# Kernel tuning notes

Hardware: AMD Instinct MI355X
Metric: run time of the kernel (lower is better)

The kernel has to match this reference:

```python
import jax, jax.numpy as jnp
import numpy as np

EMBED_DIM = 1024
NUM_HEADS = 16
HEAD_DIM = EMBED_DIM // NUM_HEADS


def setup_inputs() -> dict:
    key = jax.random.key(0)
    ks = jax.random.split(key, 9)
    B, S, D = 2, 2048, EMBED_DIM
    scale = 1.0 / np.sqrt(D)
    x = jax.random.normal(ks[0], (B, S, D), dtype=jnp.float32)
    # Linear params (torch nn.Linear: y = x @ W.T + b); store W as [out, in]
    Wq = jax.random.normal(ks[1], (D, D), dtype=jnp.float32) * scale
    bq = jnp.zeros((D,), dtype=jnp.float32)
    Wk = jax.random.normal(ks[2], (D, D), dtype=jnp.float32) * scale
    bk = jnp.zeros((D,), dtype=jnp.float32)
    Wv = jax.random.normal(ks[3], (D, D), dtype=jnp.float32) * scale
    bv = jnp.zeros((D,), dtype=jnp.float32)
    Wo = jax.random.normal(ks[4], (D, D), dtype=jnp.float32) * scale
    bo = jnp.zeros((D,), dtype=jnp.float32)
    return {"x": x, "Wq": Wq, "bq": bq, "Wk": Wk, "bk": bk,
            "Wv": Wv, "bv": bv, "Wo": Wo, "bo": bo}


def reference(x, Wq, bq, Wk, bk, Wv, bv, Wo, bo):
    B, S, D = x.shape
    H, Hd = NUM_HEADS, HEAD_DIM
    scaling = Hd ** -0.5
    # projections (torch Linear: x @ W.T + b)
    q = (x @ Wq.T + bq).reshape(B, S, H, Hd).transpose(0, 2, 1, 3)  # [B,H,S,Hd]
    k = (x @ Wk.T + bk).reshape(B, S, H, Hd).transpose(0, 2, 1, 3)
    v = (x @ Wv.T + bv).reshape(B, S, H, Hd).transpose(0, 2, 1, 3)
    # full score matrix, as in the original (no flash tiling)
    scores = jnp.einsum('bhqd,bhkd->bhqk', q, k) * scaling  # [B,H,S,S]
    attn = jax.nn.softmax(scores, axis=-1)
    # dropout is identity in eval mode
    out = jnp.einsum('bhqk,bhkd->bhqd', attn, v)  # [B,H,S,Hd]
    out = out.transpose(0, 2, 1, 3).reshape(B, S, D)
    return out @ Wo.T + bo
```

## Files before the change

### kernel.cpp

```cpp
#include <hip/hip_runtime.h>
#include <stdint.h>

typedef unsigned short u16;
typedef short short8 __attribute__((ext_vector_type(8)));
typedef short bh4 __attribute__((ext_vector_type(4)));
typedef float f32x4 __attribute__((ext_vector_type(4)));

__device__ __forceinline__ u16 f2bf_fast(float f) {
  union { float f; uint32_t u; } x;
  x.f = f;
  return (u16)((x.u + 0x8000u) >> 16);
}

__device__ __forceinline__ uint32_t pack2bf(float lo, float hi) {
  union { float f; uint32_t u; } a, b;
  a.f = lo; b.f = hi;
  return __builtin_amdgcn_perm(b.u + 0x8000u, a.u + 0x8000u, 0x07060302u);
}

__device__ __forceinline__ float bf2f(uint32_t u) {
  union { uint32_t u; float f; } x;
  x.u = u << 16;
  return x.f;
}

__device__ __forceinline__ void gload_lds16(const void* g, void* l) {
  __builtin_amdgcn_global_load_lds(
      (const __attribute__((address_space(1))) void*)g,
      (__attribute__((address_space(3))) void*)l, 16, 0, 0);
}

__device__ __forceinline__ f32x4 mfma16(short8 a, short8 b, f32x4 c) {
  return __builtin_amdgcn_mfma_f32_16x16x32_bf16(a, b, c, 0, 0, 0);
}

__device__ __forceinline__ f32x4 pv_mfma(bh4 a, bh4 b, f32x4 c) {
#if defined(__AMDGCN__) || defined(__HIP_DEVICE_COMPILE__)
  return __builtin_amdgcn_mfma_f32_16x16x16bf16_1k(a, b, c, 0, 0, 0);
#else
  (void)a; (void)b;
  return c;
#endif
}

__device__ __forceinline__ short8 ldfrag(const u16* base, int tile, int kc,
                                         int lane) {
  return *(const short8*)(base + ((((tile << 5) + kc) << 6) + lane) * 8);
}

#define QSCALE 0.18033688011112042f

__global__ void pack_all(const float* __restrict__ x, const float* __restrict__ wq,
                         const float* __restrict__ wk, const float* __restrict__ wv,
                         const float* __restrict__ wo, u16* __restrict__ xp,
                         u16* __restrict__ wp) {
  const int gi = blockIdx.x * 256 + threadIdx.x;
  const int lane = gi & 63;
  const int kc = (gi >> 6) & 31;
  const int rt = gi >> 11;
  const int col = kc * 32 + (lane >> 4) * 8;
  const float* src;
  int row;
  if (rt < 256) {
    src = x;
    row = rt * 16 + (lane & 15);
  } else {
    const int wti = rt - 256;
    const int widx = wti >> 6;
    src = (widx == 0) ? wq : (widx == 1) ? wk : (widx == 2) ? wv : wo;
    row = (wti & 63) * 16 + (lane & 15);
  }
  const float4* p = (const float4*)(src + (size_t)row * 1024 + col);
  const float4 v0 = p[0], v1 = p[1];
  uint4 o;
  o.x = pack2bf(v0.x, v0.y);
  o.y = pack2bf(v0.z, v0.w);
  o.z = pack2bf(v1.x, v1.y);
  o.w = pack2bf(v1.z, v1.w);
  u16* dst = (rt < 256) ? xp : wp;
  const int og = (rt < 256) ? gi : gi - 524288;
  ((uint4*)dst)[og] = o;
}

__global__ __launch_bounds__(256, 3) void proj_qkv(
    const u16* __restrict__ xp, const u16* __restrict__ wp,
    const float* __restrict__ bq, const float* __restrict__ bk,
    const float* __restrict__ bv, u16* __restrict__ qw, u16* __restrict__ kw,
    u16* __restrict__ vw) {
  const int gid = blockIdx.x * 4 + (threadIdx.x >> 6);
  const int lane = threadIdx.x & 63;
  const int quad = lane >> 4, l15 = lane & 15;
  const bool isQK = gid < 2048;
  int at0, bt0, bm, bn;
  const u16 *Ap, *Bp;
  if (isQK) {
    bn = gid >> 6; bm = gid & 63;
    Ap = xp; at0 = bm * 4;
    Bp = wp; bt0 = bn * 4;
  } else {
    const int h = gid - 2048;
    bn = h & 63; bm = h >> 6;
    Ap = wp; at0 = 128 + bm * 4;
    Bp = xp; bt0 = bn * 4;
  }

  f32x4 acc[4][4] = {};
  short8 af[2][4], bf[2][4];
#pragma unroll
  for (int mt = 0; mt < 4; ++mt) af[0][mt] = ldfrag(Ap, at0 + mt, 0, lane);
#pragma unroll
  for (int nt = 0; nt < 4; ++nt) bf[0][nt] = ldfrag(Bp, bt0 + nt, 0, lane);

#pragma unroll 4
  for (int kc = 0; kc < 32; ++kc) {
    const int cur = kc & 1, nxt = cur ^ 1;
    if (kc < 31) {
#pragma unroll
      for (int mt = 0; mt < 4; ++mt)
        af[nxt][mt] = ldfrag(Ap, at0 + mt, kc + 1, lane);
#pragma unroll
      for (int nt = 0; nt < 4; ++nt)
        bf[nxt][nt] = ldfrag(Bp, bt0 + nt, kc + 1, lane);
    }
#pragma unroll
    for (int mt = 0; mt < 4; ++mt)
#pragma unroll
      for (int nt = 0; nt < 4; ++nt)
        acc[mt][nt] = mfma16(af[cur][mt], bf[cur][nt], acc[mt][nt]);
  }

#pragma unroll
  for (int nt = 0; nt < 4; ++nt) {
    const int n = bn * 64 + nt * 16 + l15;
#pragma unroll
    for (int mt = 0; mt < 4; ++mt)
#pragma unroll
      for (int r = 0; r < 4; ++r) {
        const int m = bm * 64 + mt * 16 + quad * 4 + r;
        const float a = acc[mt][nt][r];
        if (isQK) {
          const bool isQ = (bn < 16);
          const int nn = isQ ? n : n - 1024;
          const float v = isQ ? (a + bq[nn]) * QSCALE : a + bk[nn];
          u16* op = isQ ? qw : kw;
          const int b = m >> 11, s = m & 2047, hh = nn >> 6, d = nn & 63;
          op[((size_t)((b * 16 + hh) * 2048 + s)) * 64 + d] = f2bf_fast(v);
        } else {
          const float v = a + bv[m];
          const int b = n >> 11, s = n & 2047;
          vw[((size_t)(b * 1024 + m)) * 2048 + s] = f2bf_fast(v);
        }
      }
  }
}

__global__ __launch_bounds__(256) void attn_kernel(
    const u16* __restrict__ Q, const u16* __restrict__ Kt,
    const u16* __restrict__ Vt, u16* __restrict__ op0, u16* __restrict__ op1,
    float* __restrict__ lp) {
  __shared__ __align__(16) u16 Sm[16384];
  const int tid = threadIdx.x, lane = tid & 63, w = tid >> 6;
  const int quad = lane >> 4, l15 = lane & 15;
  const int qt = blockIdx.x;
  const int bh = blockIdx.y >> 1;
  const int ks = blockIdx.y & 1;

  const char* Qb = (const char*)(Q + ((size_t)bh * 2048 + qt * 128) * 64);
  const char* Kb = (const char*)(Kt + ((size_t)bh * 2048 + ks * 1024) * 64);
  const char* Vb = (const char*)(Vt + (size_t)bh * 64 * 2048 + ks * 1024);

  auto stageKV = [&](int kt, int b) {
    u16* Kl = Sm + b * 4096;
    u16* Vl = Sm + 8192 + b * 4096;
#pragma unroll
    for (int i = 0; i < 2; ++i) {
      const int G = (w * 2 + i) * 64 + lane;
      const int r = G >> 3, sl = G & 7;
      gload_lds16(Kb + (size_t)(kt * 64 + r) * 128 + ((sl ^ (r & 7)) * 16),
                  &Kl[G * 8]);
      gload_lds16(Vb + (size_t)r * 4096 + kt * 128 + ((sl ^ (r & 7)) * 16),
                  &Vl[G * 8]);
    }
  };

#pragma unroll
  for (int i = 0; i < 4; ++i) {
    const int G = (w * 4 + i) * 64 + lane;
    const int row = G >> 3, sl = G & 7;
    u16* qdst = (G < 512) ? (Sm + 4096) : (Sm + 12288);
    gload_lds16(Qb + (size_t)row * 128 + ((sl ^ (row & 7)) * 16),
                &qdst[(G & 511) * 8]);
  }
  stageKV(0, 0);
  __syncthreads();

  const u16* qreg = (w < 2) ? (Sm + 4096) : (Sm + 12288);
  const int qr0 = (w & 1) * 32;
  short8 aq[2][2];
#pragma unroll
  for (int mt = 0; mt < 2; ++mt)
#pragma unroll
    for (int kc = 0; kc < 2; ++kc)
      aq[mt][kc] = *(const short8*)&qreg[(qr0 + mt * 16 + l15) * 64 +
                                         (((kc * 4 + quad) ^ (l15 & 7)) * 8)];
  __syncthreads();

  f32x4 ot[4][2] = {};
  float lsum[2] = {};

  for (int kt = 0; kt < 16; ++kt) {
    const int buf = kt & 1;
    if (kt < 15) stageKV(kt + 1, buf ^ 1);
    const u16* Kl = Sm + buf * 4096;
    const u16* Vl = Sm + 8192 + buf * 4096;

    f32x4 st[2][4] = {};
#pragma unroll
    for (int kc = 0; kc < 2; ++kc)
#pragma unroll
      for (int ntk = 0; ntk < 4; ++ntk) {
        short8 kf = *(const short8*)&Kl[(ntk * 16 + l15) * 64 +
                                        (((kc * 4 + quad) ^ (l15 & 7)) * 8)];
        st[0][ntk] = mfma16(kf, aq[0][kc], st[0][ntk]);
        st[1][ntk] = mfma16(kf, aq[1][kc], st[1][ntk]);
      }

    bh4 bp[2][4];
#pragma unroll
    for (int mt = 0; mt < 2; ++mt)
#pragma unroll
      for (int ntk = 0; ntk < 4; ++ntk) {
        const float e0 = __builtin_amdgcn_exp2f(st[mt][ntk][0]);
        const float e1 = __builtin_amdgcn_exp2f(st[mt][ntk][1]);
        const float e2 = __builtin_amdgcn_exp2f(st[mt][ntk][2]);
        const float e3 = __builtin_amdgcn_exp2f(st[mt][ntk][3]);
        lsum[mt] += (e0 + e1) + (e2 + e3);
        union { uint32_t u[2]; bh4 s; } pb;
        pb.u[0] = pack2bf(e0, e1);
        pb.u[1] = pack2bf(e2, e3);
        bp[mt][ntk] = pb.s;
      }

#pragma unroll
    for (int ntk = 0; ntk < 4; ++ntk) {
      const int swz = ((ntk * 2 + (quad >> 1)) ^ (l15 & 7)) * 8 + (quad & 1) * 4;
#pragma unroll
      for (int ntd = 0; ntd < 4; ++ntd) {
        bh4 vf = *(const bh4*)&Vl[(ntd * 16 + l15) * 64 + swz];
        ot[ntd][0] = pv_mfma(vf, bp[0][ntk], ot[ntd][0]);
        ot[ntd][1] = pv_mfma(vf, bp[1][ntk], ot[ntd][1]);
      }
    }
    if (kt < 15) __syncthreads();
  }

  const int b = bh >> 4, h = bh & 15;
  u16* op = ks ? op1 : op0;
#pragma unroll
  for (int mt = 0; mt < 2; ++mt) {
    float l = lsum[mt];
    l += __shfl_xor(l, 16);
    l += __shfl_xor(l, 32);
    const int srow = qt * 128 + w * 32 + mt * 16 + l15;
    if (quad == 0) lp[((size_t)(ks * 32 + bh)) * 2048 + srow] = l;
    const int rt = b * 128 + qt * 8 + w * 2 + mt;
#pragma unroll
    for (int ntd = 0; ntd < 4; ++ntd) {
      const int kc = h * 2 + (ntd >> 1);
      const int lnq = ((ntd & 1) * 2 + (quad >> 1)) & 3;
      const int j0 = (quad & 1) * 4;
      uint2 ov;
      ov.x = pack2bf(ot[ntd][mt][0], ot[ntd][mt][1]);
      ov.y = pack2bf(ot[ntd][mt][2], ot[ntd][mt][3]);
      *(uint2*)(op + ((size_t)((rt * 32 + kc) * 64 + lnq * 16 + l15)) * 8 + j0) = ov;
    }
  }
}

__global__ void attn_combine(const u16* __restrict__ op0,
                             const u16* __restrict__ op1,
                             const float* __restrict__ lp,
                             u16* __restrict__ awp) {
  const int g = blockIdx.x * 256 + threadIdx.x;
  const int ln = g & 63;
  const int kc = (g >> 6) & 31;
  const int rt = g >> 11;
  const int row = rt * 16 + (ln & 15);
  const int b = row >> 11, s = row & 2047;
  const int h = kc >> 1;
  const int lidx = (b * 16 + h) * 2048 + s;
  const float inv = __builtin_amdgcn_rcpf(lp[lidx] + lp[lidx + 65536]);
  const uint4 a0 = ((const uint4*)op0)[g];
  const uint4 a1 = ((const uint4*)op1)[g];
  uint4 o;
  o.x = pack2bf((bf2f(a0.x) + bf2f(a1.x)) * inv,
                (bf2f(a0.x >> 16) + bf2f(a1.x >> 16)) * inv);
  o.y = pack2bf((bf2f(a0.y) + bf2f(a1.y)) * inv,
                (bf2f(a0.y >> 16) + bf2f(a1.y >> 16)) * inv);
  o.z = pack2bf((bf2f(a0.z) + bf2f(a1.z)) * inv,
                (bf2f(a0.z >> 16) + bf2f(a1.z >> 16)) * inv);
  o.w = pack2bf((bf2f(a0.w) + bf2f(a1.w)) * inv,
                (bf2f(a0.w >> 16) + bf2f(a1.w >> 16)) * inv);
  ((uint4*)awp)[g] = o;
}

__global__ __launch_bounds__(256, 3) void out_proj(const u16* __restrict__ awp,
                                                   const u16* __restrict__ wp,
                                                   const float* __restrict__ bo,
                                                   float* __restrict__ out) {
  const int gid = blockIdx.x * 4 + (threadIdx.x >> 6);
  const int lane = threadIdx.x & 63;
  const int quad = lane >> 4, l15 = lane & 15;
  const int bm = gid & 63, bnn = gid >> 6;
  const int at0 = bm * 4, bt0 = 192 + bnn * 2;

  f32x4 acc[4][2] = {};
  short8 af[2][4], bf[2][2];
#pragma unroll
  for (int mt = 0; mt < 4; ++mt) af[0][mt] = ldfrag(awp, at0 + mt, 0, lane);
#pragma unroll
  for (int nt = 0; nt < 2; ++nt) bf[0][nt] = ldfrag(wp, bt0 + nt, 0, lane);

#pragma unroll 4
  for (int kc = 0; kc < 32; ++kc) {
    const int cur = kc & 1, nxt = cur ^ 1;
    if (kc < 31) {
#pragma unroll
      for (int mt = 0; mt < 4; ++mt)
        af[nxt][mt] = ldfrag(awp, at0 + mt, kc + 1, lane);
#pragma unroll
      for (int nt = 0; nt < 2; ++nt)
        bf[nxt][nt] = ldfrag(wp, bt0 + nt, kc + 1, lane);
    }
#pragma unroll
    for (int mt = 0; mt < 4; ++mt)
#pragma unroll
      for (int nt = 0; nt < 2; ++nt)
        acc[mt][nt] = mfma16(af[cur][mt], bf[cur][nt], acc[mt][nt]);
  }

#pragma unroll
  for (int nt = 0; nt < 2; ++nt) {
    const int n = bnn * 32 + nt * 16 + l15;
    const float bb = bo[n];
#pragma unroll
    for (int mt = 0; mt < 4; ++mt)
#pragma unroll
      for (int r = 0; r < 4; ++r) {
        const int m = bm * 64 + mt * 16 + quad * 4 + r;
        out[(size_t)m * 1024 + n] = acc[mt][nt][r] + bb;
      }
  }
}

extern "C" void kernel_launch(void* const* d_in, const int* in_sizes, int n_in,
                              void* d_out, int out_size, void* d_ws, size_t ws_size,
                              hipStream_t stream) {
  const float* x  = (const float*)d_in[0];
  const float* Wq = (const float*)d_in[1];
  const float* bq = (const float*)d_in[2];
  const float* Wk = (const float*)d_in[3];
  const float* bk = (const float*)d_in[4];
  const float* Wv = (const float*)d_in[5];
  const float* bv = (const float*)d_in[6];
  const float* Wo = (const float*)d_in[7];
  const float* bo = (const float*)d_in[8];

  const size_t M4 = (size_t)4 * 1024 * 1024;
  u16* xp  = (u16*)d_ws;
  u16* wp  = xp + M4;
  u16* qw  = wp + M4;
  u16* kw  = qw + M4;
  u16* vw  = kw + M4;
  u16* op1 = vw + M4;
  u16* awp = op1 + M4;
  float* lp = (float*)(awp + M4);
  u16* op0 = xp;

  pack_all<<<4096, 256, 0, stream>>>(x, Wq, Wk, Wv, Wo, xp, wp);

  proj_qkv<<<768, 256, 0, stream>>>(xp, wp, bq, bk, bv, qw, kw, vw);

  attn_kernel<<<dim3(16, 64), 256, 0, stream>>>(qw, kw, vw, op0, op1, lp);

  attn_combine<<<2048, 256, 0, stream>>>(op0, op1, lp, awp);

  out_proj<<<512, 256, 0, stream>>>(awp, wp, bo, (float*)d_out);
}
```

Baseline: 208.6 us.

## Use 16x16x32 MFMA for PV via lane shuffles and XCD-aware GEMM block mapping

```diff
diff --git a/kernel.cpp b/kernel.cpp
--- a/kernel.cpp
+++ b/kernel.cpp
@@ -3,7 +3,6 @@
 
 typedef unsigned short u16;
 typedef short short8 __attribute__((ext_vector_type(8)));
-typedef short bh4 __attribute__((ext_vector_type(4)));
 typedef float f32x4 __attribute__((ext_vector_type(4)));
 
 __device__ __forceinline__ u16 f2bf_fast(float f) {
@@ -32,15 +31,6 @@
 
 __device__ __forceinline__ f32x4 mfma16(short8 a, short8 b, f32x4 c) {
   return __builtin_amdgcn_mfma_f32_16x16x32_bf16(a, b, c, 0, 0, 0);
-}
-
-__device__ __forceinline__ f32x4 pv_mfma(bh4 a, bh4 b, f32x4 c) {
-#if defined(__AMDGCN__) || defined(__HIP_DEVICE_COMPILE__)
-  return __builtin_amdgcn_mfma_f32_16x16x16bf16_1k(a, b, c, 0, 0, 0);
-#else
-  (void)a; (void)b;
-  return c;
-#endif
 }
 
 __device__ __forceinline__ short8 ldfrag(const u16* base, int tile, int kc,
@@ -87,19 +77,25 @@
     const float* __restrict__ bq, const float* __restrict__ bk,
     const float* __restrict__ bv, u16* __restrict__ qw, u16* __restrict__ kw,
     u16* __restrict__ vw) {
-  const int gid = blockIdx.x * 4 + (threadIdx.x >> 6);
+  const int wv2 = threadIdx.x >> 6;
   const int lane = threadIdx.x & 63;
   const int quad = lane >> 4, l15 = lane & 15;
-  const bool isQK = gid < 2048;
+  const int xcd = blockIdx.x & 7;
+  const int bidx = blockIdx.x >> 3;
+  const int xq = xcd >> 1, xh = xcd & 1;
+  const bool isQK = bidx < 64;
   int at0, bt0, bm, bn;
   const u16 *Ap, *Bp;
   if (isQK) {
-    bn = gid >> 6; bm = gid & 63;
+    const int q = bidx;
+    bn = xh * 16 + (q & 15);
+    bm = xq * 16 + (q >> 4) * 4 + wv2;
     Ap = xp; at0 = bm * 4;
     Bp = wp; bt0 = bn * 4;
   } else {
-    const int h = gid - 2048;
-    bn = h & 63; bm = h >> 6;
+    const int v = bidx - 64;
+    bn = xq * 16 + (v & 15);
+    bm = xh * 8 + (v >> 4) * 4 + wv2;
     Ap = wp; at0 = 128 + bm * 4;
     Bp = xp; bt0 = bn * 4;
   }
@@ -164,6 +160,7 @@
   const int qt = blockIdx.x;
   const int bh = blockIdx.y >> 1;
   const int ks = blockIdx.y & 1;
+  const int sl = (l15 & 3) | ((l15 >> 1) & 4) | ((l15 << 1) & 8);
 
   const char* Qb = (const char*)(Q + ((size_t)bh * 2048 + qt * 128) * 64);
   const char* Kb = (const char*)(Kt + ((size_t)bh * 2048 + ks * 1024) * 64);
@@ -175,10 +172,10 @@
 #pragma unroll
     for (int i = 0; i < 2; ++i) {
       const int G = (w * 2 + i) * 64 + lane;
-      const int r = G >> 3, sl = G & 7;
-      gload_lds16(Kb + (size_t)(kt * 64 + r) * 128 + ((sl ^ (r & 7)) * 16),
+      const int r = G >> 3, slw = G & 7;
+      gload_lds16(Kb + (size_t)(kt * 64 + r) * 128 + ((slw ^ (r & 7)) * 16),
                   &Kl[G * 8]);
-      gload_lds16(Vb + (size_t)r * 4096 + kt * 128 + ((sl ^ (r & 7)) * 16),
+      gload_lds16(Vb + (size_t)r * 4096 + kt * 128 + ((slw ^ (r & 7)) * 16),
                   &Vl[G * 8]);
     }
   };
@@ -186,9 +183,9 @@
 #pragma unroll
   for (int i = 0; i < 4; ++i) {
     const int G = (w * 4 + i) * 64 + lane;
-    const int row = G >> 3, sl = G & 7;
+    const int row = G >> 3, slw = G & 7;
     u16* qdst = (G < 512) ? (Sm + 4096) : (Sm + 12288);
-    gload_lds16(Qb + (size_t)row * 128 + ((sl ^ (row & 7)) * 16),
+    gload_lds16(Qb + (size_t)row * 128 + ((slw ^ (row & 7)) * 16),
                 &qdst[(G & 511) * 8]);
   }
   stageKV(0, 0);
@@ -219,13 +216,13 @@
     for (int kc = 0; kc < 2; ++kc)
 #pragma unroll
       for (int ntk = 0; ntk < 4; ++ntk) {
-        short8 kf = *(const short8*)&Kl[(ntk * 16 + l15) * 64 +
-                                        (((kc * 4 + quad) ^ (l15 & 7)) * 8)];
+        short8 kf = *(const short8*)&Kl[(ntk * 16 + sl) * 64 +
+                                        (((kc * 4 + quad) ^ (sl & 7)) * 8)];
         st[0][ntk] = mfma16(kf, aq[0][kc], st[0][ntk]);
         st[1][ntk] = mfma16(kf, aq[1][kc], st[1][ntk]);
       }
 
-    bh4 bp[2][4];
+    uint2 pp[2][4];
 #pragma unroll
     for (int mt = 0; mt < 2; ++mt)
 #pragma unroll
@@ -235,22 +232,36 @@
         const float e2 = __builtin_amdgcn_exp2f(st[mt][ntk][2]);
         const float e3 = __builtin_amdgcn_exp2f(st[mt][ntk][3]);
         lsum[mt] += (e0 + e1) + (e2 + e3);
-        union { uint32_t u[2]; bh4 s; } pb;
-        pb.u[0] = pack2bf(e0, e1);
-        pb.u[1] = pack2bf(e2, e3);
-        bp[mt][ntk] = pb.s;
-      }
-
-#pragma unroll
-    for (int ntk = 0; ntk < 4; ++ntk) {
-      const int swz = ((ntk * 2 + (quad >> 1)) ^ (l15 & 7)) * 8 + (quad & 1) * 4;
+        pp[mt][ntk].x = pack2bf(e0, e1);
+        pp[mt][ntk].y = pack2bf(e2, e3);
+      }
+
+    short8 pf[2][2];
+#pragma unroll
+    for (int mt = 0; mt < 2; ++mt)
+#pragma unroll
+      for (int g = 0; g < 2; ++g) {
+        const uint2 o0 = pp[mt][2 * g], o1 = pp[mt][2 * g + 1];
+        const uint32_t x0l = __shfl_xor(o0.x, 32), x0h = __shfl_xor(o0.y, 32);
+        const uint32_t x1l = __shfl_xor(o1.x, 32), x1h = __shfl_xor(o1.y, 32);
+        union { uint32_t u[4]; short8 s; } f;
+        if (quad < 2) {
+          f.u[0] = o0.x; f.u[1] = o0.y; f.u[2] = x0l; f.u[3] = x0h;
+        } else {
+          f.u[0] = x1l; f.u[1] = x1h; f.u[2] = o1.x; f.u[3] = o1.y;
+        }
+        pf[mt][g] = f.s;
+      }
+
+#pragma unroll
+    for (int g = 0; g < 2; ++g)
 #pragma unroll
       for (int ntd = 0; ntd < 4; ++ntd) {
-        bh4 vf = *(const bh4*)&Vl[(ntd * 16 + l15) * 64 + swz];
-        ot[ntd][0] = pv_mfma(vf, bp[0][ntk], ot[ntd][0]);
-        ot[ntd][1] = pv_mfma(vf, bp[1][ntk], ot[ntd][1]);
-      }
-    }
+        short8 vf = *(const short8*)&Vl[(ntd * 16 + l15) * 64 +
+                                        (((g * 4 + quad) ^ (l15 & 7)) * 8)];
+        ot[ntd][0] = mfma16(vf, pf[0][g], ot[ntd][0]);
+        ot[ntd][1] = mfma16(vf, pf[1][g], ot[ntd][1]);
+      }
     if (kt < 15) __syncthreads();
   }
 
@@ -308,10 +319,14 @@
                                                    const u16* __restrict__ wp,
                                                    const float* __restrict__ bo,
                                                    float* __restrict__ out) {
-  const int gid = blockIdx.x * 4 + (threadIdx.x >> 6);
+  const int wv2 = threadIdx.x >> 6;
   const int lane = threadIdx.x & 63;
   const int quad = lane >> 4, l15 = lane & 15;
-  const int bm = gid & 63, bnn = gid >> 6;
+  const int xcd = blockIdx.x & 7;
+  const int bidx = blockIdx.x >> 3;
+  const int xq = xcd >> 1, xh = xcd & 1;
+  const int bnn = xh * 16 + (bidx & 15);
+  const int bm = xq * 16 + (bidx >> 4) * 4 + wv2;
   const int at0 = bm * 4, bt0 = 192 + bnn * 2;
 
   f32x4 acc[4][2] = {};
```

Measured after the change: 215.6 us. 1.03x slower.
